# Optimization experiments

Measured on AMD Instinct MI355X. Metric: run time of the kernel, lower is better.

The kernel has to match this reference:

```python
import jax, jax.numpy as jnp
import numpy as np

HIDDEN = 1024
H = 16        # num query heads
HKV = 4       # num kv heads
GROUPS = H // HKV
D = HIDDEN // H  # head_dim = 64
SW = (63, 0)  # sliding_window (left, right)
W = SW[0] + SW[1] + 1  # window length per query = 64
MAXPOS = 2048


def _sincos_table(num_pos, dim):
    # faithful to create_sinusoidal_positions (incl. final [:, :, :num_pos] slice)
    inv_freq = 1.0 / 10000 ** (np.arange(0, dim, 2, dtype=np.int32) / dim)
    freqs = np.einsum('i,j->ij', np.arange(num_pos, dtype=np.int32), inv_freq).astype(np.float32)
    emb = np.concatenate((freqs, freqs), axis=-1)
    out = np.concatenate((np.sin(emb)[:, None, :], np.cos(emb)[:, None, :]), axis=-1)
    return jnp.asarray(out[:, :, :num_pos])  # [num_pos, 1, 2*dim]

_SINCOS = _sincos_table(MAXPOS, D)


def _rotate_half(x):
    h = x.shape[-1] // 2
    return jnp.concatenate((-x[..., h:], x[..., :h]), axis=-1)


def setup_inputs() -> dict:
    key = jax.random.key(0)
    k0, k1, k2, k3, k4 = jax.random.split(key, 5)
    B, S = 1, 2048
    std = 0.02
    return {
        'hidden_states': jax.random.normal(k0, (B, S, HIDDEN), dtype=jnp.float32),
        'attention_mask': jnp.ones((B, S, 1, W), dtype=jnp.int32),
        'position_ids': jnp.arange(B * S, dtype=jnp.int32).reshape(B, S) % MAXPOS,
        'q_kernel': jax.random.normal(k1, (HIDDEN, H * D), dtype=jnp.float32) * std,
        'k_kernel': jax.random.normal(k2, (HIDDEN, HKV * D), dtype=jnp.float32) * std,
        'v_kernel': jax.random.normal(k3, (HIDDEN, HKV * D), dtype=jnp.float32) * std,
        'o_kernel': jax.random.normal(k4, (HIDDEN, HIDDEN), dtype=jnp.float32) * std,
    }


def reference(hidden_states, attention_mask, position_ids, q_kernel, k_kernel, v_kernel, o_kernel):
    B, S, _ = hidden_states.shape
    # QKV projections (no bias)
    q = (hidden_states @ q_kernel).reshape(B, S, H, D)
    k = (hidden_states @ k_kernel).reshape(B, S, HKV, D)
    v = (hidden_states @ v_kernel).reshape(B, S, HKV, D)
    # rotary embedding; sincos[pos] -> [B,S,1,2D], broadcasts over head axis
    sc = _SINCOS[position_ids]
    sin, cos = jnp.split(sc, 2, axis=-1)
    k = k * cos + _rotate_half(k) * sin
    q = q * cos + _rotate_half(q) * sin
    # GQA: repeat kv heads to match query heads
    k = jnp.repeat(k, GROUPS, axis=2)  # [B,S,H,D]
    v = jnp.repeat(v, GROUPS, axis=2)
    # sliding-window gather: each query position sees W surrounding keys
    k = jnp.pad(k, ((0, 0), SW, (0, 0), (0, 0)))
    v = jnp.pad(v, ((0, 0), SW, (0, 0), (0, 0)))
    idx = jnp.arange(W, dtype=jnp.int32)[None, :] + jnp.arange(S, dtype=jnp.int32)[:, None]  # [S,W]
    kg = k[:, idx]  # [B,S,W,H,D]
    vg = v[:, idx]
    # attention (q_len=1 per position), scores [B,S,H,W]
    scores = jnp.einsum('bshd,bswhd->bshw', q, kg) / jnp.asarray(np.sqrt(D), scores_dtype := jnp.float32)
    neg = jnp.finfo(jnp.float32).min
    m = attention_mask[:, :, 0, :][:, :, None, :]  # [B,S,1,W] broadcast over H
    bias = jnp.where(m > 0, jnp.float32(0.0), neg)
    weights = jax.nn.softmax(scores + bias, axis=-1)
    attn = jnp.einsum('bshw,bswhd->bshd', weights, vg).reshape(B, S, HIDDEN)
    return attn @ o_kernel
```

## Files before the change

### kernel.cpp

```cpp
#include <hip/hip_runtime.h>
#include <hip/hip_bf16.h>
#include <math.h>

#define S        2048
#define HIDDEN   1024
#define NH       16
#define NKV      4
#define HD       64
#define NQKV     1536
#define VW       2128

typedef _Float16 f16x8 __attribute__((ext_vector_type(8)));
typedef _Float16 f16x4 __attribute__((ext_vector_type(4)));
typedef float    f32x4 __attribute__((ext_vector_type(4)));

__device__ __forceinline__ void glds16(const void* g, void* l) {
    __builtin_amdgcn_global_load_lds((const __attribute__((address_space(1))) void*)g,
                                     (__attribute__((address_space(3))) void*)l, 16, 0, 0);
}

__global__ __launch_bounds__(256) void prep_kernel(const float* __restrict__ hs, _Float16* __restrict__ hsf16,
                                                   const float* __restrict__ wq, const float* __restrict__ wk,
                                                   const float* __restrict__ wvv, const float* __restrict__ wo,
                                                   _Float16* __restrict__ wqkvT, _Float16* __restrict__ woT,
                                                   const int* __restrict__ pos_ids, float2* __restrict__ rope_tab,
                                                   _Float16* __restrict__ vTs) {
    int bid = blockIdx.x;
    int tid = threadIdx.x;
    if (bid >= 4864) {
        int d = bid - 4864;
        if (tid < 64) vTs[(size_t)d * VW + tid] = (_Float16)0.0f;
        return;
    }
    if (bid >= 4608) {
        int idx = (bid - 4608) * 256 + tid;
        int s = idx >> 5, f = idx & 31;
        double inv = pow(10000.0, -(double)(2 * f) / 64.0);
        float ang = (float)((double)pos_ids[s] * inv);
        float sn, cs;
        sincosf(ang, &sn, &cs);
        rope_tab[idx] = make_float2(sn, cs);
        return;
    }
    if (bid >= 2560) {
        int i = (bid - 2560) * 256 + tid;
        float4 v = ((const float4*)hs)[i];
        f16x4 o = { (_Float16)v.x, (_Float16)v.y, (_Float16)v.z, (_Float16)v.w };
        *(f16x4*)(hsf16 + 4 * (size_t)i) = o;
        return;
    }
    const float* src; _Float16* dst; int Cn, b;
    if (bid < 1024)      { src = wq;  dst = wqkvT;                       Cn = 1024; b = bid; }
    else if (bid < 1280) { src = wk;  dst = wqkvT + (size_t)1024 * 1024; Cn = 256;  b = bid - 1024; }
    else if (bid < 1536) { src = wvv; dst = wqkvT + (size_t)1280 * 1024; Cn = 256;  b = bid - 1280; }
    else                 { src = wo;  dst = woT;                         Cn = 1024; b = bid - 1536; }
    int xb = Cn >> 5;
    int c0 = (b % xb) * 32;
    int r0 = (b / xb) * 32;
    __shared__ float t[32][33];
    int tx = tid & 31, ty = tid >> 5;
#pragma unroll
    for (int i = ty; i < 32; i += 8)
        t[i][tx] = src[(size_t)(r0 + i) * Cn + c0 + tx];
    __syncthreads();
#pragma unroll
    for (int i = ty; i < 32; i += 8)
        dst[(size_t)(c0 + i) * 1024 + r0 + tx] = (_Float16)t[tx][i];
}

__global__ __launch_bounds__(256) void gemm_qkv(const _Float16* __restrict__ A,
                                                const _Float16* __restrict__ BT,
                                                _Float16* __restrict__ qkv,
                                                _Float16* __restrict__ vTs,
                                                const float2* __restrict__ rope_tab) {
    const int K = HIDDEN;
    const int m0   = blockIdx.y * 128;
    const int n0   = blockIdx.x * 64;
    const int tid  = threadIdx.x;
    const int lane = tid & 63;
    const int wv   = tid >> 6;
    const int lr   = lane & 15;
    const int quad = lane >> 4;
    const int wm   = wv * 32;
    const int dr   = lane >> 3;
    const int cc   = lane & 7;

    __shared__ __align__(16) _Float16 As[128 * 64];
    __shared__ __align__(16) _Float16 Bs[64 * 64];

    f32x4 acc[2][4] = {};

    for (int k0 = 0; k0 < K; k0 += 64) {
        __syncthreads();
#pragma unroll
        for (int t = 0; t < 4; ++t) {
            int r = wv * 32 + t * 8 + dr;
            glds16(A + (size_t)(m0 + r) * K + k0 + (cc ^ (r & 7)) * 8,
                   As + (wv * 32 + t * 8) * 64);
        }
#pragma unroll
        for (int t = 0; t < 2; ++t) {
            int r = wv * 16 + t * 8 + dr;
            glds16(BT + (size_t)(n0 + r) * K + k0 + (cc ^ (r & 7)) * 8,
                   Bs + (wv * 16 + t * 8) * 64);
        }
        __syncthreads();
#pragma unroll
        for (int ks = 0; ks < 2; ++ks) {
            f16x8 a[2], b[4];
#pragma unroll
            for (int i = 0; i < 2; ++i) {
                int row = wm + i * 16 + lr;
                a[i] = *(const f16x8*)&As[row * 64 + ((ks * 4 + quad) ^ (row & 7)) * 8];
            }
#pragma unroll
            for (int j = 0; j < 4; ++j) {
                int row = j * 16 + lr;
                b[j] = *(const f16x8*)&Bs[row * 64 + ((ks * 4 + quad) ^ (row & 7)) * 8];
            }
#pragma unroll
            for (int i = 0; i < 2; ++i)
#pragma unroll
                for (int j = 0; j < 4; ++j)
                    acc[i][j] = __builtin_amdgcn_mfma_f32_16x16x32_f16(a[i], b[j], acc[i][j], 0, 0, 0);
        }
    }

    if (n0 < 1280) {
        const bool isq = (n0 < 1024);
#pragma unroll
        for (int i = 0; i < 2; ++i)
#pragma unroll
            for (int r = 0; r < 4; ++r) {
                int s = m0 + wm + i * 16 + quad * 4 + r;
                const float2* tb = rope_tab + (size_t)s * 32;
#pragma unroll
                for (int j = 0; j < 2; ++j) {
                    float2 sc = tb[j * 16 + lr];
                    float lo = acc[i][j][r], hi = acc[i][j + 2][r];
                    float nlo = lo * sc.y - hi * sc.x;
                    float nhi = hi * sc.y + lo * sc.x;
                    if (isq) { nlo *= 0.125f; nhi *= 0.125f; }
                    qkv[(size_t)s * NQKV + n0 + j * 16 + lr]      = (_Float16)nlo;
                    qkv[(size_t)s * NQKV + n0 + 32 + j * 16 + lr] = (_Float16)nhi;
                }
            }
    } else {
#pragma unroll
        for (int i = 0; i < 2; ++i)
#pragma unroll
            for (int j = 0; j < 4; ++j) {
                int d = n0 - 1280 + j * 16 + lr;
                f16x4 h = { (_Float16)acc[i][j][0], (_Float16)acc[i][j][1],
                            (_Float16)acc[i][j][2], (_Float16)acc[i][j][3] };
                *(f16x4*)(vTs + (size_t)d * VW + 64 + m0 + wm + i * 16 + quad * 4) = h;
            }
    }
}

__global__ __launch_bounds__(256) void gemm_o(const _Float16* __restrict__ A,
                                              const _Float16* __restrict__ BT,
                                              float* __restrict__ C) {
    const int K = HIDDEN, N = HIDDEN;
    const int m0   = blockIdx.y * 128;
    const int n0   = blockIdx.x * 64;
    const int tid  = threadIdx.x;
    const int lane = tid & 63;
    const int wv   = tid >> 6;
    const int lr   = lane & 15;
    const int quad = lane >> 4;
    const int wm   = (wv >> 1) * 64;
    const int wn   = (wv & 1) * 32;
    const int dr   = lane >> 3;
    const int cc   = lane & 7;

    __shared__ __align__(16) _Float16 As[128 * 64];
    __shared__ __align__(16) _Float16 Bs[64 * 64];

    f32x4 acc[4][2] = {};

    for (int k0 = 0; k0 < K; k0 += 64) {
        __syncthreads();
#pragma unroll
        for (int t = 0; t < 4; ++t) {
            int r = wv * 32 + t * 8 + dr;
            glds16(A + (size_t)(m0 + r) * K + k0 + (cc ^ (r & 7)) * 8,
                   As + (wv * 32 + t * 8) * 64);
        }
#pragma unroll
        for (int t = 0; t < 2; ++t) {
            int r = wv * 16 + t * 8 + dr;
            glds16(BT + (size_t)(n0 + r) * K + k0 + (cc ^ (r & 7)) * 8,
                   Bs + (wv * 16 + t * 8) * 64);
        }
        __syncthreads();
#pragma unroll
        for (int ks = 0; ks < 2; ++ks) {
            f16x8 a[4], b[2];
#pragma unroll
            for (int i = 0; i < 4; ++i) {
                int row = wm + i * 16 + lr;
                a[i] = *(const f16x8*)&As[row * 64 + ((ks * 4 + quad) ^ (row & 7)) * 8];
            }
#pragma unroll
            for (int j = 0; j < 2; ++j) {
                int row = wn + j * 16 + lr;
                b[j] = *(const f16x8*)&Bs[row * 64 + ((ks * 4 + quad) ^ (row & 7)) * 8];
            }
#pragma unroll
            for (int i = 0; i < 4; ++i)
#pragma unroll
                for (int j = 0; j < 2; ++j)
                    acc[i][j] = __builtin_amdgcn_mfma_f32_16x16x32_f16(a[i], b[j], acc[i][j], 0, 0, 0);
        }
    }
#pragma unroll
    for (int i = 0; i < 4; ++i)
#pragma unroll
        for (int j = 0; j < 2; ++j)
#pragma unroll
            for (int r = 0; r < 4; ++r)
                C[(size_t)(m0 + wm + i * 16 + quad * 4 + r) * N + n0 + wn + j * 16 + lr] = acc[i][j][r];
}

__global__ __launch_bounds__(256) void attn_mfma(const _Float16* __restrict__ qkv,
                                                 const _Float16* __restrict__ vTs,
                                                 const int* __restrict__ mask,
                                                 _Float16* __restrict__ attn_out) {
    const int s0   = blockIdx.x * 16;
    const int g    = blockIdx.y;
    const int tid  = threadIdx.x;
    const int lane = tid & 63;
    const int wv   = tid >> 6;
    const int h    = g * 4 + wv;
    const int lr   = lane & 15;
    const int quad = lane >> 4;

    __shared__ __align__(16) _Float16 K_lds[80 * 72];
    __shared__ __align__(16) _Float16 Vt_lds[64 * 104];
    __shared__ __align__(16) _Float16 P_lds[4][16 * 104];
    __shared__ int M_lds[1024];

    ((int4*)M_lds)[tid] = ((const int4*)(mask + s0 * 64))[tid];

    for (int c = tid; c < 640; c += 256) {
        int r = c >> 3, cl = c & 7;
        int j = s0 - 64 + r;
        f16x8 val = {};
        if (j >= 0)
            val = *(const f16x8*)(qkv + (size_t)j * NQKV + 1024 + g * 64 + cl * 8);
        *(f16x8*)&K_lds[r * 72 + cl * 8] = val;
    }
    for (int c = tid; c < 64 * 12; c += 256) {
        int d = c / 12, ch = c % 12;
        *(f16x8*)&Vt_lds[d * 104 + ch * 8] =
            *(const f16x8*)(vTs + (size_t)(g * 64 + d) * VW + s0 + ch * 8);
    }

    f16x8 qf[2];
#pragma unroll
    for (int ks = 0; ks < 2; ++ks)
        qf[ks] = *(const f16x8*)(qkv + (size_t)(s0 + lr) * NQKV + h * 64 + ks * 32 + quad * 8);
    __syncthreads();

    f32x4 sc[5];
#pragma unroll
    for (int t = 0; t < 5; ++t) {
        f32x4 a = {};
#pragma unroll
        for (int ks = 0; ks < 2; ++ks) {
            f16x8 kf = *(const f16x8*)&K_lds[(t * 16 + lr) * 72 + ks * 32 + quad * 8];
            a = __builtin_amdgcn_mfma_f32_16x16x32_f16(qf[ks], kf, a, 0, 0, 0);
        }
        sc[t] = a;
    }

#pragma unroll
    for (int t = 0; t < 5; ++t)
#pragma unroll
        for (int r = 0; r < 4; ++r) {
            int qi = quad * 4 + r;
            int w  = t * 16 + lr - 1 - qi;
            bool ok = (w >= 0) && (w < 64) && (M_lds[qi * 64 + (w & 63)] > 0);
            sc[t][r] = ok ? sc[t][r] : -1e30f;
        }

    float pr[5][4];
#pragma unroll
    for (int r = 0; r < 4; ++r) {
        float mx = -1e30f;
#pragma unroll
        for (int t = 0; t < 5; ++t) mx = fmaxf(mx, sc[t][r]);
#pragma unroll
        for (int off = 1; off < 16; off <<= 1) mx = fmaxf(mx, __shfl_xor(mx, off));
        float sum = 0.f;
#pragma unroll
        for (int t = 0; t < 5; ++t) { float e = __expf(sc[t][r] - mx); pr[t][r] = e; sum += e; }
#pragma unroll
        for (int off = 1; off < 16; off <<= 1) sum += __shfl_xor(sum, off);
        float rs = 1.0f / sum;
#pragma unroll
        for (int t = 0; t < 5; ++t) pr[t][r] *= rs;
    }

    _Float16* myP = P_lds[wv];
    {
        f16x4 z = {};
        *(f16x4*)&myP[lr * 104 + 80 + quad * 4] = z;
    }
#pragma unroll
    for (int t = 0; t < 5; ++t)
#pragma unroll
        for (int r = 0; r < 4; ++r)
            myP[(quad * 4 + r) * 104 + t * 16 + lr] = (_Float16)pr[t][r];
    __syncthreads();

    f32x4 oacc[4] = {};
#pragma unroll
    for (int ks = 0; ks < 3; ++ks) {
        f16x8 pf = *(const f16x8*)&myP[lr * 104 + ks * 32 + quad * 8];
#pragma unroll
        for (int t = 0; t < 4; ++t) {
            f16x8 vf = *(const f16x8*)&Vt_lds[(t * 16 + lr) * 104 + ks * 32 + quad * 8];
            oacc[t] = __builtin_amdgcn_mfma_f32_16x16x32_f16(pf, vf, oacc[t], 0, 0, 0);
        }
    }
#pragma unroll
    for (int t = 0; t < 4; ++t)
#pragma unroll
        for (int r = 0; r < 4; ++r)
            attn_out[(size_t)(s0 + quad * 4 + r) * HIDDEN + h * 64 + t * 16 + lr] = (_Float16)oacc[t][r];
}

extern "C" void kernel_launch(void* const* d_in, const int* in_sizes, int n_in,
                              void* d_out, int out_size, void* d_ws, size_t ws_size,
                              hipStream_t stream) {
    const float* hs      = (const float*)d_in[0];
    const int*   mask    = (const int*)  d_in[1];
    const int*   pos_ids = (const int*)  d_in[2];
    const float* wq      = (const float*)d_in[3];
    const float* wk      = (const float*)d_in[4];
    const float* wvv     = (const float*)d_in[5];
    const float* wo      = (const float*)d_in[6];
    float* out = (float*)d_out;

    char* ws = (char*)d_ws;
    _Float16* wqkvT   = (_Float16*)(ws + 0);
    _Float16* woT     = (_Float16*)(ws + (3u << 20));
    _Float16* hsf16   = (_Float16*)(ws + (5u << 20));
    _Float16* qkvf16  = (_Float16*)(ws + (9u << 20));
    _Float16* attnf16 = (_Float16*)(ws + (15u << 20));
    _Float16* vTs     = (_Float16*)(ws + (19u << 20));
    float2*   ropeTab = (float2*)  (ws + (21u << 20));

    prep_kernel<<<5120, 256, 0, stream>>>(hs, hsf16, wq, wk, wvv, wo, wqkvT, woT,
                                          pos_ids, ropeTab, vTs);
    gemm_qkv<<<dim3(NQKV / 64, S / 128), 256, 0, stream>>>(hsf16, wqkvT, qkvf16, vTs, ropeTab);
    attn_mfma<<<dim3(S / 16, NKV), 256, 0, stream>>>(qkvf16, vTs, mask, attnf16);
    gemm_o<<<dim3(HIDDEN / 64, S / 128), 256, 0, stream>>>(attnf16, woT, out);
}
```

Before: 116.3 us.

## Fuse QKV GEMM, attention and output GEMM into a persistent grid-barrier kernel

Replaces the three launches (QKV GEMM, attention, O GEMM) with one persistent 512-block kernel. Software grid barriers built on an atomic counter separate the phases. The QKV weight columns are permuted at prep time so each wave's rope pairs land in its own accumulator tiles, which allows 64x64 tiles. This removes launch gaps and per-kernel tail effects, but it depends on all 512 blocks being co-resident, adds spin-wait barrier cost, and uses smaller GEMM tiles.

```diff
diff --git a/kernel.cpp b/kernel.cpp
--- a/kernel.cpp
+++ b/kernel.cpp
@@ -9,6 +9,7 @@
 #define HD       64
 #define NQKV     1536
 #define VW       2128
+#define GRID     512
 
 typedef _Float16 f16x8 __attribute__((ext_vector_type(8)));
 typedef _Float16 f16x4 __attribute__((ext_vector_type(4)));
@@ -17,6 +18,11 @@
 __device__ __forceinline__ void glds16(const void* g, void* l) {
     __builtin_amdgcn_global_load_lds((const __attribute__((address_space(1))) void*)g,
                                      (__attribute__((address_space(3))) void*)l, 16, 0, 0);
+}
+
+__device__ __host__ __forceinline__ int ropePerm(int d) {
+    int t = d & 48;
+    return (t == 16 || t == 32) ? (d ^ 48) : d;
 }
 
 __global__ __launch_bounds__(256) void prep_kernel(const float* __restrict__ hs, _Float16* __restrict__ hsf16,
@@ -24,9 +30,10 @@
                                                    const float* __restrict__ wvv, const float* __restrict__ wo,
                                                    _Float16* __restrict__ wqkvT, _Float16* __restrict__ woT,
                                                    const int* __restrict__ pos_ids, float2* __restrict__ rope_tab,
-                                                   _Float16* __restrict__ vTs) {
+                                                   _Float16* __restrict__ vTs, int* __restrict__ bar) {
     int bid = blockIdx.x;
     int tid = threadIdx.x;
+    if (bid == 0 && tid == 0) bar[0] = 0;
     if (bid >= 4864) {
         int d = bid - 4864;
         if (tid < 64) vTs[(size_t)d * VW + tid] = (_Float16)0.0f;
@@ -49,11 +56,11 @@
         *(f16x4*)(hsf16 + 4 * (size_t)i) = o;
         return;
     }
-    const float* src; _Float16* dst; int Cn, b;
-    if (bid < 1024)      { src = wq;  dst = wqkvT;                       Cn = 1024; b = bid; }
-    else if (bid < 1280) { src = wk;  dst = wqkvT + (size_t)1024 * 1024; Cn = 256;  b = bid - 1024; }
-    else if (bid < 1536) { src = wvv; dst = wqkvT + (size_t)1280 * 1024; Cn = 256;  b = bid - 1280; }
-    else                 { src = wo;  dst = woT;                         Cn = 1024; b = bid - 1536; }
+    const float* src; _Float16* dst; int Cn, b; bool prm;
+    if (bid < 1024)      { src = wq;  dst = wqkvT;                       Cn = 1024; b = bid;        prm = true;  }
+    else if (bid < 1280) { src = wk;  dst = wqkvT + (size_t)1024 * 1024; Cn = 256;  b = bid - 1024; prm = true;  }
+    else if (bid < 1536) { src = wvv; dst = wqkvT + (size_t)1280 * 1024; Cn = 256;  b = bid - 1280; prm = false; }
+    else                 { src = wo;  dst = woT;                         Cn = 1024; b = bid - 1536; prm = false; }
     int xb = Cn >> 5;
     int c0 = (b % xb) * 32;
     int r0 = (b / xb) * 32;
@@ -64,272 +71,250 @@
         t[i][tx] = src[(size_t)(r0 + i) * Cn + c0 + tx];
     __syncthreads();
 #pragma unroll
-    for (int i = ty; i < 32; i += 8)
-        dst[(size_t)(c0 + i) * 1024 + r0 + tx] = (_Float16)t[tx][i];
-}
-
-__global__ __launch_bounds__(256) void gemm_qkv(const _Float16* __restrict__ A,
-                                                const _Float16* __restrict__ BT,
-                                                _Float16* __restrict__ qkv,
-                                                _Float16* __restrict__ vTs,
-                                                const float2* __restrict__ rope_tab) {
-    const int K = HIDDEN;
-    const int m0   = blockIdx.y * 128;
-    const int n0   = blockIdx.x * 64;
+    for (int i = ty; i < 32; i += 8) {
+        int n = c0 + i;
+        int np = prm ? ((n & ~63) | ropePerm(n & 63)) : n;
+        dst[(size_t)np * 1024 + r0 + tx] = (_Float16)t[tx][i];
+    }
+}
+
+__device__ __forceinline__ void grid_barrier(int* cnt, int target) {
+    __syncthreads();
+    if (threadIdx.x == 0) {
+        __threadfence();
+        __hip_atomic_fetch_add(cnt, 1, __ATOMIC_ACQ_REL, __HIP_MEMORY_SCOPE_AGENT);
+        while (__hip_atomic_load(cnt, __ATOMIC_ACQUIRE, __HIP_MEMORY_SCOPE_AGENT) < target)
+            __builtin_amdgcn_s_sleep(2);
+    }
+    __syncthreads();
+    __threadfence();
+}
+
+__global__ __launch_bounds__(256, 2) void mega_kernel(const _Float16* __restrict__ A,
+                                                      const _Float16* __restrict__ BT,
+                                                      _Float16* __restrict__ qkv,
+                                                      _Float16* __restrict__ vTs,
+                                                      const float2* __restrict__ rope_tab,
+                                                      const int* __restrict__ mask,
+                                                      _Float16* __restrict__ attnW,
+                                                      const _Float16* __restrict__ woT,
+                                                      float* __restrict__ out,
+                                                      int* __restrict__ bar) {
+    __shared__ __align__(16) char smem[42240];
+    const int bid  = blockIdx.x;
     const int tid  = threadIdx.x;
     const int lane = tid & 63;
     const int wv   = tid >> 6;
     const int lr   = lane & 15;
     const int quad = lane >> 4;
-    const int wm   = wv * 32;
     const int dr   = lane >> 3;
     const int cc   = lane & 7;
-
-    __shared__ __align__(16) _Float16 As[128 * 64];
-    __shared__ __align__(16) _Float16 Bs[64 * 64];
-
-    f32x4 acc[2][4] = {};
-
-    for (int k0 = 0; k0 < K; k0 += 64) {
+    const int wm   = (wv >> 1) * 32;
+    const int wn   = (wv & 1) * 32;
+
+    _Float16* As = (_Float16*)smem;
+    _Float16* Bs = (_Float16*)(smem + 8192);
+
+    for (int t = bid; t < 768; t += GRID) {
+        const int bx = t % 24, by = t / 24;
+        const int m0 = by * 64, n0 = bx * 64;
+        f32x4 acc[2][2] = {};
+        for (int k0 = 0; k0 < 1024; k0 += 64) {
+            __syncthreads();
+#pragma unroll
+            for (int u = 0; u < 2; ++u) {
+                int r = wv * 16 + u * 8 + dr;
+                glds16(A  + (size_t)(m0 + r) * 1024 + k0 + (cc ^ (r & 7)) * 8, As + (wv * 16 + u * 8) * 64);
+                glds16(BT + (size_t)(n0 + r) * 1024 + k0 + (cc ^ (r & 7)) * 8, Bs + (wv * 16 + u * 8) * 64);
+            }
+            __syncthreads();
+#pragma unroll
+            for (int ks = 0; ks < 2; ++ks) {
+                f16x8 a[2], b[2];
+#pragma unroll
+                for (int i = 0; i < 2; ++i) {
+                    int row = wm + i * 16 + lr;
+                    a[i] = *(const f16x8*)&As[row * 64 + ((ks * 4 + quad) ^ (row & 7)) * 8];
+                }
+#pragma unroll
+                for (int j = 0; j < 2; ++j) {
+                    int row = wn + j * 16 + lr;
+                    b[j] = *(const f16x8*)&Bs[row * 64 + ((ks * 4 + quad) ^ (row & 7)) * 8];
+                }
+#pragma unroll
+                for (int i = 0; i < 2; ++i)
+#pragma unroll
+                    for (int j = 0; j < 2; ++j)
+                        acc[i][j] = __builtin_amdgcn_mfma_f32_16x16x32_f16(a[i], b[j], acc[i][j], 0, 0, 0);
+            }
+        }
+        if (n0 < 1280) {
+            const bool isq = (n0 < 1024);
+            const int  f   = (wn >> 1) + lr;
+#pragma unroll
+            for (int i = 0; i < 2; ++i)
+#pragma unroll
+                for (int r = 0; r < 4; ++r) {
+                    int s = m0 + wm + i * 16 + quad * 4 + r;
+                    float2 scv = rope_tab[(size_t)s * 32 + f];
+                    float lo = acc[i][0][r], hi = acc[i][1][r];
+                    float nlo = lo * scv.y - hi * scv.x;
+                    float nhi = hi * scv.y + lo * scv.x;
+                    if (isq) { nlo *= 0.125f; nhi *= 0.125f; }
+                    qkv[(size_t)s * NQKV + n0 + wn + lr]      = (_Float16)nlo;
+                    qkv[(size_t)s * NQKV + n0 + wn + 16 + lr] = (_Float16)nhi;
+                }
+        } else {
+#pragma unroll
+            for (int i = 0; i < 2; ++i)
+#pragma unroll
+                for (int j = 0; j < 2; ++j) {
+                    int d = n0 - 1280 + wn + j * 16 + lr;
+                    f16x4 h = { (_Float16)acc[i][j][0], (_Float16)acc[i][j][1],
+                                (_Float16)acc[i][j][2], (_Float16)acc[i][j][3] };
+                    *(f16x4*)(vTs + (size_t)d * VW + 64 + m0 + wm + i * 16 + quad * 4) = h;
+                }
+        }
+    }
+    grid_barrier(bar, GRID);
+
+    {
+        _Float16* K_lds  = (_Float16*)smem;
+        _Float16* Vt_lds = (_Float16*)(smem + 11520);
+        _Float16* P_all  = (_Float16*)(smem + 24832);
+        int*      M_lds  = (int*)     (smem + 38144);
+        const int s0 = (bid & 127) * 16;
+        const int g  = bid >> 7;
+        const int h  = g * 4 + wv;
+
+        ((int4*)M_lds)[tid] = ((const int4*)(mask + s0 * 64))[tid];
+        for (int c = tid; c < 640; c += 256) {
+            int r = c >> 3, cl = c & 7;
+            int j = s0 - 64 + r;
+            f16x8 val = {};
+            if (j >= 0)
+                val = *(const f16x8*)(qkv + (size_t)j * NQKV + 1024 + g * 64 + cl * 8);
+            *(f16x8*)&K_lds[r * 72 + cl * 8] = val;
+        }
+        for (int c = tid; c < 64 * 12; c += 256) {
+            int d = c / 12, ch = c % 12;
+            *(f16x8*)&Vt_lds[d * 104 + ch * 8] =
+                *(const f16x8*)(vTs + (size_t)(g * 64 + d) * VW + s0 + ch * 8);
+        }
+        f16x8 qf[2];
+#pragma unroll
+        for (int ks = 0; ks < 2; ++ks)
+            qf[ks] = *(const f16x8*)(qkv + (size_t)(s0 + lr) * NQKV + h * 64 + ks * 32 + quad * 8);
         __syncthreads();
-#pragma unroll
-        for (int t = 0; t < 4; ++t) {
-            int r = wv * 32 + t * 8 + dr;
-            glds16(A + (size_t)(m0 + r) * K + k0 + (cc ^ (r & 7)) * 8,
-                   As + (wv * 32 + t * 8) * 64);
-        }
-#pragma unroll
-        for (int t = 0; t < 2; ++t) {
-            int r = wv * 16 + t * 8 + dr;
-            glds16(BT + (size_t)(n0 + r) * K + k0 + (cc ^ (r & 7)) * 8,
-                   Bs + (wv * 16 + t * 8) * 64);
-        }
+
+        f32x4 sc[5];
+#pragma unroll
+        for (int t = 0; t < 5; ++t) {
+            f32x4 a = {};
+#pragma unroll
+            for (int ks = 0; ks < 2; ++ks) {
+                f16x8 kf = *(const f16x8*)&K_lds[(t * 16 + lr) * 72 + ks * 32 + quad * 8];
+                a = __builtin_amdgcn_mfma_f32_16x16x32_f16(qf[ks], kf, a, 0, 0, 0);
+            }
+            sc[t] = a;
+        }
+#pragma unroll
+        for (int t = 0; t < 5; ++t)
+#pragma unroll
+            for (int r = 0; r < 4; ++r) {
+                int qi = quad * 4 + r;
+                int w  = t * 16 + lr - 1 - qi;
+                bool ok = (w >= 0) && (w < 64) && (M_lds[qi * 64 + (w & 63)] > 0);
+                sc[t][r] = ok ? sc[t][r] : -1e30f;
+            }
+        float pr[5][4];
+#pragma unroll
+        for (int r = 0; r < 4; ++r) {
+            float mx = -1e30f;
+#pragma unroll
+            for (int t = 0; t < 5; ++t) mx = fmaxf(mx, sc[t][r]);
+#pragma unroll
+            for (int off = 1; off < 16; off <<= 1) mx = fmaxf(mx, __shfl_xor(mx, off));
+            float sum = 0.f;
+#pragma unroll
+            for (int t = 0; t < 5; ++t) { float e = __expf(sc[t][r] - mx); pr[t][r] = e; sum += e; }
+#pragma unroll
+            for (int off = 1; off < 16; off <<= 1) sum += __shfl_xor(sum, off);
+            float rs = 1.0f / sum;
+#pragma unroll
+            for (int t = 0; t < 5; ++t) pr[t][r] *= rs;
+        }
+        _Float16* myP = P_all + wv * 16 * 104;
+        {
+            f16x4 z = {};
+            *(f16x4*)&myP[lr * 104 + 80 + quad * 4] = z;
+        }
+#pragma unroll
+        for (int t = 0; t < 5; ++t)
+#pragma unroll
+            for (int r = 0; r < 4; ++r)
+                myP[(quad * 4 + r) * 104 + t * 16 + lr] = (_Float16)pr[t][r];
         __syncthreads();
-#pragma unroll
-        for (int ks = 0; ks < 2; ++ks) {
-            f16x8 a[2], b[4];
-#pragma unroll
-            for (int i = 0; i < 2; ++i) {
-                int row = wm + i * 16 + lr;
-                a[i] = *(const f16x8*)&As[row * 64 + ((ks * 4 + quad) ^ (row & 7)) * 8];
-            }
-#pragma unroll
-            for (int j = 0; j < 4; ++j) {
-                int row = j * 16 + lr;
-                b[j] = *(const f16x8*)&Bs[row * 64 + ((ks * 4 + quad) ^ (row & 7)) * 8];
-            }
-#pragma unroll
-            for (int i = 0; i < 2; ++i)
-#pragma unroll
-                for (int j = 0; j < 4; ++j)
-                    acc[i][j] = __builtin_amdgcn_mfma_f32_16x16x32_f16(a[i], b[j], acc[i][j], 0, 0, 0);
-        }
-    }
-
-    if (n0 < 1280) {
-        const bool isq = (n0 < 1024);
+
+        f32x4 oacc[4] = {};
+#pragma unroll
+        for (int ks = 0; ks < 3; ++ks) {
+            f16x8 pf = *(const f16x8*)&myP[lr * 104 + ks * 32 + quad * 8];
+#pragma unroll
+            for (int t = 0; t < 4; ++t) {
+                f16x8 vf = *(const f16x8*)&Vt_lds[(t * 16 + lr) * 104 + ks * 32 + quad * 8];
+                oacc[t] = __builtin_amdgcn_mfma_f32_16x16x32_f16(pf, vf, oacc[t], 0, 0, 0);
+            }
+        }
+#pragma unroll
+        for (int t = 0; t < 4; ++t)
+#pragma unroll
+            for (int r = 0; r < 4; ++r)
+                attnW[(size_t)(s0 + quad * 4 + r) * HIDDEN + h * 64 + t * 16 + lr] = (_Float16)oacc[t][r];
+    }
+    grid_barrier(bar, 2 * GRID);
+
+    {
+        const int bx = bid % 16, by = bid / 16;
+        const int m0 = by * 64, n0 = bx * 64;
+        f32x4 acc[2][2] = {};
+        for (int k0 = 0; k0 < 1024; k0 += 64) {
+            __syncthreads();
+#pragma unroll
+            for (int u = 0; u < 2; ++u) {
+                int r = wv * 16 + u * 8 + dr;
+                glds16(attnW + (size_t)(m0 + r) * 1024 + k0 + (cc ^ (r & 7)) * 8, As + (wv * 16 + u * 8) * 64);
+                glds16(woT   + (size_t)(n0 + r) * 1024 + k0 + (cc ^ (r & 7)) * 8, Bs + (wv * 16 + u * 8) * 64);
+            }
+            __syncthreads();
+#pragma unroll
+            for (int ks = 0; ks < 2; ++ks) {
+                f16x8 a[2], b[2];
+#pragma unroll
+                for (int i = 0; i < 2; ++i) {
+                    int row = wm + i * 16 + lr;
+                    a[i] = *(const f16x8*)&As[row * 64 + ((ks * 4 + quad) ^ (row & 7)) * 8];
+                }
+#pragma unroll
+                for (int j = 0; j < 2; ++j) {
+                    int row = wn + j * 16 + lr;
+                    b[j] = *(const f16x8*)&Bs[row * 64 + ((ks * 4 + quad) ^ (row & 7)) * 8];
+                }
+#pragma unroll
+                for (int i = 0; i < 2; ++i)
+#pragma unroll
+                    for (int j = 0; j < 2; ++j)
+                        acc[i][j] = __builtin_amdgcn_mfma_f32_16x16x32_f16(a[i], b[j], acc[i][j], 0, 0, 0);
+            }
+        }
 #pragma unroll
         for (int i = 0; i < 2; ++i)
 #pragma unroll
-            for (int r = 0; r < 4; ++r) {
-                int s = m0 + wm + i * 16 + quad * 4 + r;
-                const float2* tb = rope_tab + (size_t)s * 32;
-#pragma unroll
-                for (int j = 0; j < 2; ++j) {
-                    float2 sc = tb[j * 16 + lr];
-                    float lo = acc[i][j][r], hi = acc[i][j + 2][r];
-                    float nlo = lo * sc.y - hi * sc.x;
-                    float nhi = hi * sc.y + lo * sc.x;
-                    if (isq) { nlo *= 0.125f; nhi *= 0.125f; }
-                    qkv[(size_t)s * NQKV + n0 + j * 16 + lr]      = (_Float16)nlo;
-                    qkv[(size_t)s * NQKV + n0 + 32 + j * 16 + lr] = (_Float16)nhi;
-                }
-            }
-    } else {
-#pragma unroll
-        for (int i = 0; i < 2; ++i)
-#pragma unroll
-            for (int j = 0; j < 4; ++j) {
-                int d = n0 - 1280 + j * 16 + lr;
-                f16x4 h = { (_Float16)acc[i][j][0], (_Float16)acc[i][j][1],
-                            (_Float16)acc[i][j][2], (_Float16)acc[i][j][3] };
-                *(f16x4*)(vTs + (size_t)d * VW + 64 + m0 + wm + i * 16 + quad * 4) = h;
-            }
-    }
-}
-
-__global__ __launch_bounds__(256) void gemm_o(const _Float16* __restrict__ A,
-                                              const _Float16* __restrict__ BT,
-                                              float* __restrict__ C) {
-    const int K = HIDDEN, N = HIDDEN;
-    const int m0   = blockIdx.y * 128;
-    const int n0   = blockIdx.x * 64;
-    const int tid  = threadIdx.x;
-    const int lane = tid & 63;
-    const int wv   = tid >> 6;
-    const int lr   = lane & 15;
-    const int quad = lane >> 4;
-    const int wm   = (wv >> 1) * 64;
-    const int wn   = (wv & 1) * 32;
-    const int dr   = lane >> 3;
-    const int cc   = lane & 7;
-
-    __shared__ __align__(16) _Float16 As[128 * 64];
-    __shared__ __align__(16) _Float16 Bs[64 * 64];
-
-    f32x4 acc[4][2] = {};
-
-    for (int k0 = 0; k0 < K; k0 += 64) {
-        __syncthreads();
-#pragma unroll
-        for (int t = 0; t < 4; ++t) {
-            int r = wv * 32 + t * 8 + dr;
-            glds16(A + (size_t)(m0 + r) * K + k0 + (cc ^ (r & 7)) * 8,
-                   As + (wv * 32 + t * 8) * 64);
-        }
-#pragma unroll
-        for (int t = 0; t < 2; ++t) {
-            int r = wv * 16 + t * 8 + dr;
-            glds16(BT + (size_t)(n0 + r) * K + k0 + (cc ^ (r & 7)) * 8,
-                   Bs + (wv * 16 + t * 8) * 64);
-        }
-        __syncthreads();
-#pragma unroll
-        for (int ks = 0; ks < 2; ++ks) {
-            f16x8 a[4], b[2];
-#pragma unroll
-            for (int i = 0; i < 4; ++i) {
-                int row = wm + i * 16 + lr;
-                a[i] = *(const f16x8*)&As[row * 64 + ((ks * 4 + quad) ^ (row & 7)) * 8];
-            }
-#pragma unroll
-            for (int j = 0; j < 2; ++j) {
-                int row = wn + j * 16 + lr;
-                b[j] = *(const f16x8*)&Bs[row * 64 + ((ks * 4 + quad) ^ (row & 7)) * 8];
-            }
-#pragma unroll
-            for (int i = 0; i < 4; ++i)
-#pragma unroll
-                for (int j = 0; j < 2; ++j)
-                    acc[i][j] = __builtin_amdgcn_mfma_f32_16x16x32_f16(a[i], b[j], acc[i][j], 0, 0, 0);
-        }
-    }
-#pragma unroll
-    for (int i = 0; i < 4; ++i)
-#pragma unroll
-        for (int j = 0; j < 2; ++j)
-#pragma unroll
-            for (int r = 0; r < 4; ++r)
-                C[(size_t)(m0 + wm + i * 16 + quad * 4 + r) * N + n0 + wn + j * 16 + lr] = acc[i][j][r];
-}
-
-__global__ __launch_bounds__(256) void attn_mfma(const _Float16* __restrict__ qkv,
-                                                 const _Float16* __restrict__ vTs,
-                                                 const int* __restrict__ mask,
-                                                 _Float16* __restrict__ attn_out) {
-    const int s0   = blockIdx.x * 16;
-    const int g    = blockIdx.y;
-    const int tid  = threadIdx.x;
-    const int lane = tid & 63;
-    const int wv   = tid >> 6;
-    const int h    = g * 4 + wv;
-    const int lr   = lane & 15;
-    const int quad = lane >> 4;
-
-    __shared__ __align__(16) _Float16 K_lds[80 * 72];
-    __shared__ __align__(16) _Float16 Vt_lds[64 * 104];
-    __shared__ __align__(16) _Float16 P_lds[4][16 * 104];
-    __shared__ int M_lds[1024];
-
-    ((int4*)M_lds)[tid] = ((const int4*)(mask + s0 * 64))[tid];
-
-    for (int c = tid; c < 640; c += 256) {
-        int r = c >> 3, cl = c & 7;
-        int j = s0 - 64 + r;
-        f16x8 val = {};
-        if (j >= 0)
-            val = *(const f16x8*)(qkv + (size_t)j * NQKV + 1024 + g * 64 + cl * 8);
-        *(f16x8*)&K_lds[r * 72 + cl * 8] = val;
-    }
-    for (int c = tid; c < 64 * 12; c += 256) {
-        int d = c / 12, ch = c % 12;
-        *(f16x8*)&Vt_lds[d * 104 + ch * 8] =
-            *(const f16x8*)(vTs + (size_t)(g * 64 + d) * VW + s0 + ch * 8);
-    }
-
-    f16x8 qf[2];
-#pragma unroll
-    for (int ks = 0; ks < 2; ++ks)
-        qf[ks] = *(const f16x8*)(qkv + (size_t)(s0 + lr) * NQKV + h * 64 + ks * 32 + quad * 8);
-    __syncthreads();
-
-    f32x4 sc[5];
-#pragma unroll
-    for (int t = 0; t < 5; ++t) {
-        f32x4 a = {};
-#pragma unroll
-        for (int ks = 0; ks < 2; ++ks) {
-            f16x8 kf = *(const f16x8*)&K_lds[(t * 16 + lr) * 72 + ks * 32 + quad * 8];
-            a = __builtin_amdgcn_mfma_f32_16x16x32_f16(qf[ks], kf, a, 0, 0, 0);
-        }
-        sc[t] = a;
-    }
-
-#pragma unroll
-    for (int t = 0; t < 5; ++t)
-#pragma unroll
-        for (int r = 0; r < 4; ++r) {
-            int qi = quad * 4 + r;
-            int w  = t * 16 + lr - 1 - qi;
-            bool ok = (w >= 0) && (w < 64) && (M_lds[qi * 64 + (w & 63)] > 0);
-            sc[t][r] = ok ? sc[t][r] : -1e30f;
-        }
-
-    float pr[5][4];
-#pragma unroll
-    for (int r = 0; r < 4; ++r) {
-        float mx = -1e30f;
-#pragma unroll
-        for (int t = 0; t < 5; ++t) mx = fmaxf(mx, sc[t][r]);
-#pragma unroll
-        for (int off = 1; off < 16; off <<= 1) mx = fmaxf(mx, __shfl_xor(mx, off));
-        float sum = 0.f;
-#pragma unroll
-        for (int t = 0; t < 5; ++t) { float e = __expf(sc[t][r] - mx); pr[t][r] = e; sum += e; }
-#pragma unroll
-        for (int off = 1; off < 16; off <<= 1) sum += __shfl_xor(sum, off);
-        float rs = 1.0f / sum;
-#pragma unroll
-        for (int t = 0; t < 5; ++t) pr[t][r] *= rs;
-    }
-
-    _Float16* myP = P_lds[wv];
-    {
-        f16x4 z = {};
-        *(f16x4*)&myP[lr * 104 + 80 + quad * 4] = z;
-    }
-#pragma unroll
-    for (int t = 0; t < 5; ++t)
-#pragma unroll
-        for (int r = 0; r < 4; ++r)
-            myP[(quad * 4 + r) * 104 + t * 16 + lr] = (_Float16)pr[t][r];
-    __syncthreads();
-
-    f32x4 oacc[4] = {};
-#pragma unroll
-    for (int ks = 0; ks < 3; ++ks) {
-        f16x8 pf = *(const f16x8*)&myP[lr * 104 + ks * 32 + quad * 8];
-#pragma unroll
-        for (int t = 0; t < 4; ++t) {
-            f16x8 vf = *(const f16x8*)&Vt_lds[(t * 16 + lr) * 104 + ks * 32 + quad * 8];
-            oacc[t] = __builtin_amdgcn_mfma_f32_16x16x32_f16(pf, vf, oacc[t], 0, 0, 0);
-        }
-    }
-#pragma unroll
-    for (int t = 0; t < 4; ++t)
-#pragma unroll
-        for (int r = 0; r < 4; ++r)
-            attn_out[(size_t)(s0 + quad * 4 + r) * HIDDEN + h * 64 + t * 16 + lr] = (_Float16)oacc[t][r];
+            for (int j = 0; j < 2; ++j)
+#pragma unroll
+                for (int r = 0; r < 4; ++r)
+                    out[(size_t)(m0 + wm + i * 16 + quad * 4 + r) * 1024 + n0 + wn + j * 16 + lr] = acc[i][j][r];
+    }
 }
 
 extern "C" void kernel_launch(void* const* d_in, const int* in_sizes, int n_in,
@@ -352,10 +337,10 @@
     _Float16* attnf16 = (_Float16*)(ws + (15u << 20));
     _Float16* vTs     = (_Float16*)(ws + (19u << 20));
     float2*   ropeTab = (float2*)  (ws + (21u << 20));
+    int*      bar     = (int*)     (ws + (22u << 20));
 
     prep_kernel<<<5120, 256, 0, stream>>>(hs, hsf16, wq, wk, wvv, wo, wqkvT, woT,
-                                          pos_ids, ropeTab, vTs);
-    gemm_qkv<<<dim3(NQKV / 64, S / 128), 256, 0, stream>>>(hsf16, wqkvT, qkvf16, vTs, ropeTab);
-    attn_mfma<<<dim3(S / 16, NKV), 256, 0, stream>>>(qkvf16, vTs, mask, attnf16);
-    gemm_o<<<dim3(HIDDEN / 64, S / 128), 256, 0, stream>>>(attnf16, woT, out);
-}
+                                          pos_ids, ropeTab, vTs, bar);
+    mega_kernel<<<GRID, 256, 0, stream>>>(hsf16, wqkvT, qkvf16, vTs, ropeTab,
+                                          mask, attnf16, woT, out, bar);
+}
```

Result: slower. 312.5 us (+168.8%).
